# Kernel tuning notes

Hardware: AMD Instinct MI355X
Metric: run time of the kernel (lower is better)

The kernel has to match this reference:

```python
import jax, jax.numpy as jnp
import numpy as np

GRID = 0.5
NG = 48
NC = 16  # output channels
CHUNK = 256  # atoms per scan step (bounds peak memory)
E2 = float(np.exp(2.0))
# order matches pro_keys ['O','C','N','S'] with vdw_dic
VDW = jnp.array([1.52, 1.7, 1.55, 1.8], dtype=jnp.float32)


def setup_inputs() -> dict:
    key = jax.random.key(0)
    k1, k2, k3 = jax.random.split(key, 3)
    N = 2048
    coords = jax.random.uniform(k1, (N, 3), dtype=jnp.float32) * (NG * GRID)  # [0, 24)
    ch_idx = jax.random.randint(k2, (N,), 0, 4, dtype=jnp.int32)
    fg = jax.random.randint(k3, (N,), 0, 16, dtype=jnp.int32)
    return {"coords": coords, "ch_idx": ch_idx, "fg": fg}


def _channel_weights(ch_idx, fg):
    # base element channel 0..3
    w = jax.nn.one_hot(ch_idx, NC, dtype=jnp.float32)
    # fg routing: 14 -> +ch4 +ch5; 15 -> +ch6 +ch9; 12/13 -> nothing; else -> +ch(fg+4)
    c1 = jnp.where(fg == 14, 4, jnp.where(fg == 15, 6, fg + 4))
    c1 = jnp.where((fg == 12) | (fg == 13), -1, c1)  # one_hot(-1) == zeros
    c2 = jnp.where(fg == 14, 5, jnp.where(fg == 15, 9, -1))
    return w + jax.nn.one_hot(c1, NC, dtype=jnp.float32) + jax.nn.one_hot(c2, NC, dtype=jnp.float32)


def _grid_forward(coords, r, w):
    # coords [N,3], r [N] vdw radii, w [N,16] channel weights -> [16,48,48,48]
    gx = GRID * jnp.arange(NG, dtype=jnp.float32)  # grid point coordinates
    nchunk = coords.shape[0] // CHUNK
    coords_c = coords.reshape(nchunk, CHUNK, 3)
    r_c = r.reshape(nchunk, CHUNK)
    w_c = w.reshape(nchunk, CHUNK, NC)

    def body(acc, args):
        c, rr, ww = args  # [CHUNK,3], [CHUNK], [CHUNK,16]
        dx2 = (c[:, 0, None] - gx) ** 2  # [CHUNK,48]
        dy2 = (c[:, 1, None] - gx) ** 2
        dz2 = (c[:, 2, None] - gx) ** 2
        d2 = dx2[:, :, None, None] + dy2[:, None, :, None] + dz2[:, None, None, :]  # [CHUNK,48,48,48]
        d = jnp.sqrt(d2)
        r_ = rr[:, None, None, None]
        r2 = r_ * r_
        f1 = jnp.exp(-2.0 * d2 / r2)
        f2 = 4.0 * d2 / (E2 * r2) - 12.0 * d / (E2 * r_) + 9.0 / E2
        val = jnp.where(d < r_, f1, jnp.where(d < 1.5 * r_, f2, 0.0))
        acc = acc + jnp.einsum('nc,nxyz->cxyz', ww, val)
        return acc, None

    out, _ = jax.lax.scan(body, jnp.zeros((NC, NG, NG, NG), jnp.float32), (coords_c, r_c, w_c))
    return out


def reference(coords, ch_idx, fg):
    r = VDW[ch_idx]
    w = _channel_weights(ch_idx, fg)
    return _grid_forward(coords, r, w)
```

## Files before the change

### kernel.cpp

```cpp
#include <hip/hip_runtime.h>

#define NG 48
#define NC 16
#define NPTS (NG * NG * NG)
#define E2F 7.3890561f
#define NINE_OVER_E2 1.2180175f

#define BR 4
#define SEGCAP 48

__device__ __constant__ float c_vdw[4] = {1.52f, 1.7f, 1.55f, 1.8f};

__global__ void prep_kernel(const float* __restrict__ coords,
                            const int* __restrict__ ch_idx,
                            const int* __restrict__ fg,
                            float4* __restrict__ atomA,
                            float4* __restrict__ atomB, int natoms)
{
    const int i = blockIdx.x * blockDim.x + threadIdx.x;
    if (i >= natoms) return;
    const float x = coords[3 * i + 0];
    const float y = coords[3 * i + 1];
    const float z = coords[3 * i + 2];
    const int ci = ch_idx[i];
    const int f  = fg[i];
    const float r  = c_vdw[ci];
    const float r2 = r * r;
    int c1 = (f == 14) ? 4 : ((f == 15) ? 6 : f + 4);
    if (f == 12 || f == 13) c1 = -1;
    const int c2 = (f == 14) ? 5 : ((f == 15) ? 9 : -1);
    int mask = 1 << ci;
    if (c1 >= 0) mask |= 1 << c1;
    if (c2 >= 0) mask |= 1 << c2;
    atomA[i] = make_float4(x, y, z, 1.5f * r);
    atomB[i] = make_float4(-2.0f / r2, 4.0f / (E2F * r2),
                           12.0f / (E2F * r), __int_as_float(mask));
}

__global__ __launch_bounds__(256)
void density_kernel(const float4* __restrict__ atomA,
                    const float4* __restrict__ atomB,
                    float* __restrict__ out, int natoms)
{
    __shared__ float4 sA[4 * SEGCAP];
    __shared__ float4 sB[4 * SEGCAP];
    __shared__ int sCnt[4];
    __shared__ float sRed[4][NC][64];

    const int t = threadIdx.x;
    const int w = t >> 6;
    const int l = t & 63;
    const int bz = blockIdx.x, by = blockIdx.y, bx = blockIdx.z;

    const int tz = l & 3, ty = (l >> 2) & 3, tx = l >> 4;
    const int gx = bx * BR + tx, gy = by * BR + ty, gz = bz * BR + tz;
    const float px = gx * 0.5f, py = gy * 0.5f, pz = gz * 0.5f;

    const float blox = bx * 2.0f, bhix = blox + 1.5f;
    const float bloy = by * 2.0f, bhiy = bloy + 1.5f;
    const float bloz = bz * 2.0f, bhiz = bloz + 1.5f;

    const int quarter = (natoms + 3) >> 2;
    const int a0 = w * quarter;
    const int a1 = min(a0 + quarter, natoms);
    int myCnt = 0;
    for (int base = a0; base < a1; base += 64) {
        const int a = base + l;
        float4 pA;
        bool pred = false;
        if (a < a1) {
            pA = atomA[a];
            const float cut = pA.w;
            const float ddx = fmaxf(fmaxf(blox - pA.x, pA.x - bhix), 0.0f);
            const float ddy = fmaxf(fmaxf(bloy - pA.y, pA.y - bhiy), 0.0f);
            const float ddz = fmaxf(fmaxf(bloz - pA.z, pA.z - bhiz), 0.0f);
            pred = fmaf(ddx, ddx, fmaf(ddy, ddy, ddz * ddz)) < cut * cut;
        }
        const unsigned long long m = __ballot(pred);
        if (pred) {
            const int o = myCnt + __popcll(m & ((1ull << l) - 1ull));
            if (o < SEGCAP) {
                sA[w * SEGCAP + o] = pA;
                sB[w * SEGCAP + o] = atomB[a];
            }
        }
        myCnt += __popcll(m);
    }
    if (l == 0) sCnt[w] = (myCnt > SEGCAP) ? SEGCAP : myCnt;
    __syncthreads();

    const int c0 = sCnt[0], c1 = sCnt[1], c2 = sCnt[2], c3 = sCnt[3];

    float acc[NC];
    #pragma unroll
    for (int c = 0; c < NC; ++c) acc[c] = 0.0f;

    #pragma unroll 1
    for (int s = 0; s < 4; ++s) {
        const int cs = (s == 0) ? c0 : (s == 1) ? c1 : (s == 2) ? c2 : c3;
        const int segbase = s * SEGCAP;
        #pragma unroll 2
        for (int i = w; i < cs; i += 4) {
            const float4 A = sA[segbase + i];
            const float4 B = sB[segbase + i];
            const float dx = px - A.x;
            const float dy = py - A.y;
            const float dz = pz - A.z;
            const float d2 = fmaf(dx, dx, fmaf(dy, dy, dz * dz));
            const float cut2 = A.w * A.w;
            if (d2 < cut2) {
                const float r2 = cut2 * (4.0f / 9.0f);
                const float d  = sqrtf(d2);
                const float f1 = __expf(B.x * d2);
                const float f2 = fmaf(B.y, d2, fmaf(-B.z, d, NINE_OVER_E2));
                const float val = (d2 < r2) ? f1 : f2;
                const int chan = __builtin_amdgcn_readfirstlane(__float_as_int(B.w));
                #pragma unroll
                for (int c = 0; c < NC; ++c)
                    if (chan & (1 << c)) acc[c] += val;
            }
        }
    }

    #pragma unroll
    for (int c = 0; c < NC; ++c) sRed[w][c][l] = acc[c];
    __syncthreads();

    const int pbase = (gx * NG + gy) * NG + gz;
    #pragma unroll
    for (int k = 0; k < 4; ++k) {
        const int c = w * 4 + k;
        const float s = sRed[0][c][l] + sRed[1][c][l] +
                        sRed[2][c][l] + sRed[3][c][l];
        out[c * NPTS + pbase] = s;
    }
}

extern "C" void kernel_launch(void* const* d_in, const int* in_sizes, int n_in,
                              void* d_out, int out_size, void* d_ws, size_t ws_size,
                              hipStream_t stream) {
    (void)n_in; (void)ws_size; (void)out_size;
    const float* coords = (const float*)d_in[0];
    const int* ch = (const int*)d_in[1];
    const int* fgp = (const int*)d_in[2];
    float* out = (float*)d_out;
    const int natoms = in_sizes[0] / 3;

    float4* atomA = (float4*)d_ws;
    float4* atomB = atomA + natoms;

    prep_kernel<<<(natoms + 255) / 256, 256, 0, stream>>>(coords, ch, fgp, atomA, atomB, natoms);
    dim3 grid(NG / BR, NG / BR, NG / BR);
    density_kernel<<<grid, 256, 0, stream>>>(atomA, atomB, out, natoms);
}
```

Measured before the change: 23.50 us.

## Retile density kernel to 2x2x16 blocks with 8 waves and LDS atomic accumulation

Each block now covers a 2x2x16 grid-point tile, and 512 threads (8 waves) split the atom culling and the accumulation. Per-channel register accumulators are replaced by LDS atomicAdds into per-wave channel slots, applied only to the set bits of the channel mask. The per-atom distance branch becomes a select, and exp2 uses a constant prescaled by log2(e). The goal is cheaper accumulation and better occupancy. The cost is LDS atomic traffic, wasted math for atoms outside the cutoff, and a tighter SEGCAP that could truncate candidate lists for elongated tiles.

```diff
diff --git a/kernel.cpp b/kernel.cpp
--- a/kernel.cpp
+++ b/kernel.cpp
@@ -5,9 +5,10 @@
 #define NPTS (NG * NG * NG)
 #define E2F 7.3890561f
 #define NINE_OVER_E2 1.2180175f
+#define LOG2E 1.44269504f
 
-#define BR 4
-#define SEGCAP 48
+#define W 8
+#define SEGCAP 28
 
 __device__ __constant__ float c_vdw[4] = {1.52f, 1.7f, 1.55f, 1.8f};
 
@@ -33,74 +34,78 @@
     if (c1 >= 0) mask |= 1 << c1;
     if (c2 >= 0) mask |= 1 << c2;
     atomA[i] = make_float4(x, y, z, 1.5f * r);
-    atomB[i] = make_float4(-2.0f / r2, 4.0f / (E2F * r2),
-                           12.0f / (E2F * r), __int_as_float(mask));
+    atomB[i] = make_float4(-2.0f * LOG2E / r2,
+                           4.0f / (E2F * r2),
+                           12.0f / (E2F * r),
+                           __int_as_float(mask));
 }
 
-__global__ __launch_bounds__(256)
+__global__ __launch_bounds__(512, 8)
 void density_kernel(const float4* __restrict__ atomA,
                     const float4* __restrict__ atomB,
                     float* __restrict__ out, int natoms)
 {
-    __shared__ float4 sA[4 * SEGCAP];
-    __shared__ float4 sB[4 * SEGCAP];
-    __shared__ int sCnt[4];
-    __shared__ float sRed[4][NC][64];
+    __shared__ float4 sA[W * SEGCAP];
+    __shared__ float4 sB[W * SEGCAP];
+    __shared__ float sAcc[W][NC][64];
+    __shared__ int sCnt[W];
 
     const int t = threadIdx.x;
     const int w = t >> 6;
     const int l = t & 63;
     const int bz = blockIdx.x, by = blockIdx.y, bx = blockIdx.z;
 
-    const int tz = l & 3, ty = (l >> 2) & 3, tx = l >> 4;
-    const int gx = bx * BR + tx, gy = by * BR + ty, gz = bz * BR + tz;
-    const float px = gx * 0.5f, py = gy * 0.5f, pz = gz * 0.5f;
+    {
+        float4* p = (float4*)sAcc;
+        p[t]        = make_float4(0.f, 0.f, 0.f, 0.f);
+        p[t + 512]  = make_float4(0.f, 0.f, 0.f, 0.f);
+        p[t + 1024] = make_float4(0.f, 0.f, 0.f, 0.f);
+        p[t + 1536] = make_float4(0.f, 0.f, 0.f, 0.f);
+    }
 
-    const float blox = bx * 2.0f, bhix = blox + 1.5f;
-    const float bloy = by * 2.0f, bhiy = bloy + 1.5f;
-    const float bloz = bz * 2.0f, bhiz = bloz + 1.5f;
+    const float blox = bx * 1.0f, bhix = blox + 0.5f;
+    const float bloy = by * 1.0f, bhiy = bloy + 0.5f;
+    const float bloz = bz * 8.0f, bhiz = bloz + 7.5f;
 
-    const int quarter = (natoms + 3) >> 2;
-    const int a0 = w * quarter;
-    const int a1 = min(a0 + quarter, natoms);
-    int myCnt = 0;
+    const int chunk = (natoms + W - 1) / W;
+    const int a0 = w * chunk;
+    const int a1 = min(a0 + chunk, natoms);
+    int cnt = 0;
+    #pragma unroll 2
     for (int base = a0; base < a1; base += 64) {
         const int a = base + l;
         float4 pA;
         bool pred = false;
         if (a < a1) {
             pA = atomA[a];
-            const float cut = pA.w;
             const float ddx = fmaxf(fmaxf(blox - pA.x, pA.x - bhix), 0.0f);
             const float ddy = fmaxf(fmaxf(bloy - pA.y, pA.y - bhiy), 0.0f);
             const float ddz = fmaxf(fmaxf(bloz - pA.z, pA.z - bhiz), 0.0f);
-            pred = fmaf(ddx, ddx, fmaf(ddy, ddy, ddz * ddz)) < cut * cut;
+            pred = fmaf(ddx, ddx, fmaf(ddy, ddy, ddz * ddz)) < pA.w * pA.w;
         }
         const unsigned long long m = __ballot(pred);
         if (pred) {
-            const int o = myCnt + __popcll(m & ((1ull << l) - 1ull));
+            const int o = cnt + __popcll(m & ((1ull << l) - 1ull));
             if (o < SEGCAP) {
                 sA[w * SEGCAP + o] = pA;
                 sB[w * SEGCAP + o] = atomB[a];
             }
         }
-        myCnt += __popcll(m);
+        cnt += __popcll(m);
     }
-    if (l == 0) sCnt[w] = (myCnt > SEGCAP) ? SEGCAP : myCnt;
+    if (l == 0) sCnt[w] = (cnt > SEGCAP) ? SEGCAP : cnt;
     __syncthreads();
 
-    const int c0 = sCnt[0], c1 = sCnt[1], c2 = sCnt[2], c3 = sCnt[3];
+    const int tz = l & 15, ty = (l >> 4) & 1, tx = l >> 5;
+    const float px = (bx * 2 + tx) * 0.5f;
+    const float py = (by * 2 + ty) * 0.5f;
+    const float pz = (bz * 16 + tz) * 0.5f;
 
-    float acc[NC];
-    #pragma unroll
-    for (int c = 0; c < NC; ++c) acc[c] = 0.0f;
-
-    #pragma unroll 1
-    for (int s = 0; s < 4; ++s) {
-        const int cs = (s == 0) ? c0 : (s == 1) ? c1 : (s == 2) ? c2 : c3;
+    float* const accw = &sAcc[w][0][l];
+    for (int s = 0; s < W; ++s) {
+        const int cs = sCnt[s];
         const int segbase = s * SEGCAP;
-        #pragma unroll 2
-        for (int i = w; i < cs; i += 4) {
+        for (int i = (w + s) & 7; i < cs; i += W) {
             const float4 A = sA[segbase + i];
             const float4 B = sB[segbase + i];
             const float dx = px - A.x;
@@ -108,31 +113,41 @@
             const float dz = pz - A.z;
             const float d2 = fmaf(dx, dx, fmaf(dy, dy, dz * dz));
             const float cut2 = A.w * A.w;
-            if (d2 < cut2) {
-                const float r2 = cut2 * (4.0f / 9.0f);
-                const float d  = sqrtf(d2);
-                const float f1 = __expf(B.x * d2);
-                const float f2 = fmaf(B.y, d2, fmaf(-B.z, d, NINE_OVER_E2));
-                const float val = (d2 < r2) ? f1 : f2;
-                const int chan = __builtin_amdgcn_readfirstlane(__float_as_int(B.w));
-                #pragma unroll
-                for (int c = 0; c < NC; ++c)
-                    if (chan & (1 << c)) acc[c] += val;
+            const float r2 = cut2 * (4.0f / 9.0f);
+            const float d  = sqrtf(d2);
+            const float f1 = exp2f(B.x * d2);
+            const float f2 = fmaf(B.y, d2, fmaf(-B.z, d, NINE_OVER_E2));
+            float val = (d2 < r2) ? f1 : f2;
+            val = (d2 < cut2) ? val : 0.0f;
+            int chan = __builtin_amdgcn_readfirstlane(__float_as_int(B.w));
+            int c0 = __builtin_ctz(chan);
+            atomicAdd(accw + c0 * 64, val);
+            chan &= chan - 1;
+            if (chan) {
+                const int c1 = __builtin_ctz(chan);
+                atomicAdd(accw + c1 * 64, val);
+                chan &= chan - 1;
+                if (chan) {
+                    const int c2 = __builtin_ctz(chan);
+                    atomicAdd(accw + c2 * 64, val);
+                }
             }
         }
     }
+    __syncthreads();
 
     #pragma unroll
-    for (int c = 0; c < NC; ++c) sRed[w][c][l] = acc[c];
-    __syncthreads();
-
-    const int pbase = (gx * NG + gy) * NG + gz;
-    #pragma unroll
-    for (int k = 0; k < 4; ++k) {
-        const int c = w * 4 + k;
-        const float s = sRed[0][c][l] + sRed[1][c][l] +
-                        sRed[2][c][l] + sRed[3][c][l];
-        out[c * NPTS + pbase] = s;
+    for (int j = 0; j < 2; ++j) {
+        const int idx = t + j * 512;
+        const int c  = idx >> 6;
+        const int ll = idx & 63;
+        float sum = 0.0f;
+        #pragma unroll
+        for (int s = 0; s < W; ++s) sum += sAcc[s][c][ll];
+        const int gz = bz * 16 + (ll & 15);
+        const int gy = by * 2 + ((ll >> 4) & 1);
+        const int gx = bx * 2 + (ll >> 5);
+        out[c * NPTS + (gx * NG + gy) * NG + gz] = sum;
     }
 }
 
@@ -150,6 +165,6 @@
     float4* atomB = atomA + natoms;
 
     prep_kernel<<<(natoms + 255) / 256, 256, 0, stream>>>(coords, ch, fgp, atomA, atomB, natoms);
-    dim3 grid(NG / BR, NG / BR, NG / BR);
-    density_kernel<<<grid, 256, 0, stream>>>(atomA, atomB, out, natoms);
+    dim3 grid(NG / 16, NG / 2, NG / 2);
+    density_kernel<<<grid, 512, 0, stream>>>(atomA, atomB, out, natoms);
 }
```

Result: slower. 61.96 us (+163.7%).

## Bin atoms into 27 super-block lists so density blocks scan few candidates

Applied to the files above, without the earlier changes.

Adds a build kernel that computes atom parameters and bins atoms into 27 spatial super-blocks (8 Å cubes, with cutoff overlap), each capped at 512 entries. Density blocks then scan only their super-block's list instead of all 2048 atoms, which cuts global loads and the cull work per block. It also folds log2(e) into the exponent coefficient so exp2f can be used, and reuses the staging shared memory as the reduction buffer. Risks are silent truncation if a super-block holds more than 512 atoms, and a build kernel of only 27 blocks that re-reads all atoms in each block.

```diff
diff --git a/kernel.cpp b/kernel.cpp
--- a/kernel.cpp
+++ b/kernel.cpp
@@ -5,91 +5,150 @@
 #define NPTS (NG * NG * NG)
 #define E2F 7.3890561f
 #define NINE_OVER_E2 1.2180175f
+#define LOG2E 1.44269504f
 
 #define BR 4
 #define SEGCAP 48
+#define SBCAP 512
+#define MAXATOMS 2048
 
 __device__ __constant__ float c_vdw[4] = {1.52f, 1.7f, 1.55f, 1.8f};
 
-__global__ void prep_kernel(const float* __restrict__ coords,
-                            const int* __restrict__ ch_idx,
-                            const int* __restrict__ fg,
-                            float4* __restrict__ atomA,
-                            float4* __restrict__ atomB, int natoms)
-{
-    const int i = blockIdx.x * blockDim.x + threadIdx.x;
-    if (i >= natoms) return;
-    const float x = coords[3 * i + 0];
-    const float y = coords[3 * i + 1];
-    const float z = coords[3 * i + 2];
-    const int ci = ch_idx[i];
-    const int f  = fg[i];
-    const float r  = c_vdw[ci];
+__device__ __forceinline__ void atom_params(int ci, int f, float r,
+                                            float& b0, float& b1, float& b2, int& mask) {
     const float r2 = r * r;
     int c1 = (f == 14) ? 4 : ((f == 15) ? 6 : f + 4);
     if (f == 12 || f == 13) c1 = -1;
     const int c2 = (f == 14) ? 5 : ((f == 15) ? 9 : -1);
-    int mask = 1 << ci;
+    mask = 1 << ci;
     if (c1 >= 0) mask |= 1 << c1;
     if (c2 >= 0) mask |= 1 << c2;
-    atomA[i] = make_float4(x, y, z, 1.5f * r);
-    atomB[i] = make_float4(-2.0f / r2, 4.0f / (E2F * r2),
-                           12.0f / (E2F * r), __int_as_float(mask));
+    b0 = -2.0f * LOG2E / r2;
+    b1 = 4.0f / (E2F * r2);
+    b2 = 12.0f / (E2F * r);
+}
+
+__global__ __launch_bounds__(1024)
+void build_kernel(const float* __restrict__ coords,
+                  const int* __restrict__ ch_idx,
+                  const int* __restrict__ fg,
+                  float4* __restrict__ segA, float4* __restrict__ segB,
+                  int* __restrict__ counts, int natoms)
+{
+    __shared__ float sx[MAXATOMS], sy[MAXATOMS], sz[MAXATOMS], scut[MAXATOMS];
+    __shared__ float sb0[MAXATOMS], sb1[MAXATOMS], sb2[MAXATOMS], sb3[MAXATOMS];
+    __shared__ int sCnt[16];
+
+    const int t = threadIdx.x, w = t >> 6, l = t & 63;
+    const int n = min(natoms, MAXATOMS);
+
+    for (int i = t; i < n; i += 1024) {
+        const float x = coords[3 * i], y = coords[3 * i + 1], z = coords[3 * i + 2];
+        const int ci = ch_idx[i], f = fg[i];
+        const float r = c_vdw[ci];
+        float b0, b1, b2; int mask;
+        atom_params(ci, f, r, b0, b1, b2, mask);
+        sx[i] = x; sy[i] = y; sz[i] = z; scut[i] = 1.5f * r;
+        sb0[i] = b0; sb1[i] = b1; sb2[i] = b2; sb3[i] = __int_as_float(mask);
+    }
+    __syncthreads();
+
+    const int sb = blockIdx.x;
+    const int sbx = sb / 9, sby = (sb / 3) % 3, sbz = sb % 3;
+    const float lox = sbx * 8.0f, hix = lox + 7.5f;
+    const float loy = sby * 8.0f, hiy = loy + 7.5f;
+    const float loz = sbz * 8.0f, hiz = loz + 7.5f;
+
+    int runTot = 0;
+    for (int base = 0; base < n; base += 1024) {
+        const int a = base + t;
+        bool pred = false;
+        float ax = 0.f, ay = 0.f, az = 0.f, cut = 0.f;
+        if (a < n) {
+            ax = sx[a]; ay = sy[a]; az = sz[a]; cut = scut[a];
+            const float ddx = fmaxf(fmaxf(lox - ax, ax - hix), 0.f);
+            const float ddy = fmaxf(fmaxf(loy - ay, ay - hiy), 0.f);
+            const float ddz = fmaxf(fmaxf(loz - az, az - hiz), 0.f);
+            pred = fmaf(ddx, ddx, fmaf(ddy, ddy, ddz * ddz)) < cut * cut;
+        }
+        const unsigned long long m = __ballot(pred);
+        if (l == 0) sCnt[w] = __popcll(m);
+        __syncthreads();
+        int ofs = runTot, tot = 0;
+        #pragma unroll
+        for (int w2 = 0; w2 < 16; ++w2) {
+            const int c = sCnt[w2];
+            if (w2 < w) ofs += c;
+            tot += c;
+        }
+        if (pred) {
+            const int o = ofs + __popcll(m & ((1ull << l) - 1ull));
+            if (o < SBCAP) {
+                segA[sb * SBCAP + o] = make_float4(ax, ay, az, cut);
+                segB[sb * SBCAP + o] = make_float4(sb0[a], sb1[a], sb2[a], sb3[a]);
+            }
+        }
+        runTot += tot;
+        __syncthreads();
+    }
+    if (t == 0) counts[sb] = min(runTot, SBCAP);
 }
 
 __global__ __launch_bounds__(256)
-void density_kernel(const float4* __restrict__ atomA,
-                    const float4* __restrict__ atomB,
-                    float* __restrict__ out, int natoms)
+void density_kernel(const float4* __restrict__ segA,
+                    const float4* __restrict__ segB,
+                    const int* __restrict__ counts,
+                    float* __restrict__ out)
 {
-    __shared__ float4 sA[4 * SEGCAP];
-    __shared__ float4 sB[4 * SEGCAP];
+    __shared__ __align__(16) unsigned char smem[16384];
     __shared__ int sCnt[4];
-    __shared__ float sRed[4][NC][64];
-
-    const int t = threadIdx.x;
-    const int w = t >> 6;
-    const int l = t & 63;
+    float4* const sA = (float4*)smem;
+    float4* const sB = sA + 4 * SEGCAP;
+    float (*const sRed)[64] = (float (*)[64])smem;
+
+    const int t = threadIdx.x, w = t >> 6, l = t & 63;
     const int bz = blockIdx.x, by = blockIdx.y, bx = blockIdx.z;
-
-    const int tz = l & 3, ty = (l >> 2) & 3, tx = l >> 4;
-    const int gx = bx * BR + tx, gy = by * BR + ty, gz = bz * BR + tz;
-    const float px = gx * 0.5f, py = gy * 0.5f, pz = gz * 0.5f;
 
     const float blox = bx * 2.0f, bhix = blox + 1.5f;
     const float bloy = by * 2.0f, bhiy = bloy + 1.5f;
     const float bloz = bz * 2.0f, bhiz = bloz + 1.5f;
 
-    const int quarter = (natoms + 3) >> 2;
-    const int a0 = w * quarter;
-    const int a1 = min(a0 + quarter, natoms);
+    const int sb = ((bx >> 2) * 3 + (by >> 2)) * 3 + (bz >> 2);
+    const int cnt_sb = counts[sb];
+    const float4* const srcA = segA + sb * SBCAP;
+    const float4* const srcB = segB + sb * SBCAP;
+
+    const int q = (cnt_sb + 3) >> 2;
+    const int i0 = w * q, i1 = min(i0 + q, cnt_sb);
     int myCnt = 0;
-    for (int base = a0; base < a1; base += 64) {
-        const int a = base + l;
-        float4 pA;
+    for (int base = i0; base < i1; base += 64) {
+        const int idx = base + l;
         bool pred = false;
-        if (a < a1) {
-            pA = atomA[a];
-            const float cut = pA.w;
-            const float ddx = fmaxf(fmaxf(blox - pA.x, pA.x - bhix), 0.0f);
-            const float ddy = fmaxf(fmaxf(bloy - pA.y, pA.y - bhiy), 0.0f);
-            const float ddz = fmaxf(fmaxf(bloz - pA.z, pA.z - bhiz), 0.0f);
-            pred = fmaf(ddx, ddx, fmaf(ddy, ddy, ddz * ddz)) < cut * cut;
+        float4 pA, pB;
+        if (idx < i1) {
+            pA = srcA[idx];
+            pB = srcB[idx];
+            const float ddx = fmaxf(fmaxf(blox - pA.x, pA.x - bhix), 0.f);
+            const float ddy = fmaxf(fmaxf(bloy - pA.y, pA.y - bhiy), 0.f);
+            const float ddz = fmaxf(fmaxf(bloz - pA.z, pA.z - bhiz), 0.f);
+            pred = fmaf(ddx, ddx, fmaf(ddy, ddy, ddz * ddz)) < pA.w * pA.w;
         }
         const unsigned long long m = __ballot(pred);
         if (pred) {
             const int o = myCnt + __popcll(m & ((1ull << l) - 1ull));
-            if (o < SEGCAP) {
-                sA[w * SEGCAP + o] = pA;
-                sB[w * SEGCAP + o] = atomB[a];
-            }
+            if (o < SEGCAP) { sA[w * SEGCAP + o] = pA; sB[w * SEGCAP + o] = pB; }
         }
         myCnt += __popcll(m);
     }
-    if (l == 0) sCnt[w] = (myCnt > SEGCAP) ? SEGCAP : myCnt;
+    if (l == 0) sCnt[w] = min(myCnt, SEGCAP);
     __syncthreads();
 
     const int c0 = sCnt[0], c1 = sCnt[1], c2 = sCnt[2], c3 = sCnt[3];
+
+    const int tz = l & 3, ty = (l >> 2) & 3, tx = l >> 4;
+    const float px = (bx * BR + tx) * 0.5f;
+    const float py = (by * BR + ty) * 0.5f;
+    const float pz = (bz * BR + tz) * 0.5f;
 
     float acc[NC];
     #pragma unroll
@@ -111,7 +170,7 @@
             if (d2 < cut2) {
                 const float r2 = cut2 * (4.0f / 9.0f);
                 const float d  = sqrtf(d2);
-                const float f1 = __expf(B.x * d2);
+                const float f1 = exp2f(B.x * d2);
                 const float f2 = fmaf(B.y, d2, fmaf(-B.z, d, NINE_OVER_E2));
                 const float val = (d2 < r2) ? f1 : f2;
                 const int chan = __builtin_amdgcn_readfirstlane(__float_as_int(B.w));
@@ -121,35 +180,152 @@
             }
         }
     }
-
-    #pragma unroll
-    for (int c = 0; c < NC; ++c) sRed[w][c][l] = acc[c];
-    __syncthreads();
-
+    __syncthreads();
+
+    #pragma unroll
+    for (int c = 0; c < NC; ++c) sRed[w * NC + c][l] = acc[c];
+    __syncthreads();
+
+    const int gx = bx * BR + tx, gy = by * BR + ty, gz = bz * BR + tz;
     const int pbase = (gx * NG + gy) * NG + gz;
     #pragma unroll
     for (int k = 0; k < 4; ++k) {
         const int c = w * 4 + k;
-        const float s = sRed[0][c][l] + sRed[1][c][l] +
-                        sRed[2][c][l] + sRed[3][c][l];
+        const float s = sRed[0 * NC + c][l] + sRed[1 * NC + c][l] +
+                        sRed[2 * NC + c][l] + sRed[3 * NC + c][l];
         out[c * NPTS + pbase] = s;
+    }
+}
+
+__global__ void prep_kernel(const float* __restrict__ coords,
+                            const int* __restrict__ ch_idx,
+                            const int* __restrict__ fg,
+                            float4* __restrict__ atomA,
+                            float4* __restrict__ atomB, int natoms)
+{
+    const int i = blockIdx.x * blockDim.x + threadIdx.x;
+    if (i >= natoms) return;
+    const int ci = ch_idx[i], f = fg[i];
+    const float r = c_vdw[ci];
+    float b0, b1, b2; int mask;
+    atom_params(ci, f, r, b0, b1, b2, mask);
+    atomA[i] = make_float4(coords[3 * i], coords[3 * i + 1], coords[3 * i + 2], 1.5f * r);
+    atomB[i] = make_float4(b0, b1, b2, __int_as_float(mask));
+}
+
+__global__ __launch_bounds__(256)
+void density_scan_kernel(const float4* __restrict__ atomA,
+                         const float4* __restrict__ atomB,
+                         float* __restrict__ out, int natoms)
+{
+    __shared__ __align__(16) unsigned char smem[16384];
+    __shared__ int sCnt[4];
+    float4* const sA = (float4*)smem;
+    float4* const sB = sA + 4 * SEGCAP;
+    float (*const sRed)[64] = (float (*)[64])smem;
+
+    const int t = threadIdx.x, w = t >> 6, l = t & 63;
+    const int bz = blockIdx.x, by = blockIdx.y, bx = blockIdx.z;
+
+    const float blox = bx * 2.0f, bhix = blox + 1.5f;
+    const float bloy = by * 2.0f, bhiy = bloy + 1.5f;
+    const float bloz = bz * 2.0f, bhiz = bloz + 1.5f;
+
+    const int quarter = (natoms + 3) >> 2;
+    const int a0 = w * quarter, a1 = min(a0 + quarter, natoms);
+    int myCnt = 0;
+    for (int base = a0; base < a1; base += 64) {
+        const int a = base + l;
+        bool pred = false; float4 pA;
+        if (a < a1) {
+            pA = atomA[a];
+            const float ddx = fmaxf(fmaxf(blox - pA.x, pA.x - bhix), 0.f);
+            const float ddy = fmaxf(fmaxf(bloy - pA.y, pA.y - bhiy), 0.f);
+            const float ddz = fmaxf(fmaxf(bloz - pA.z, pA.z - bhiz), 0.f);
+            pred = fmaf(ddx, ddx, fmaf(ddy, ddy, ddz * ddz)) < pA.w * pA.w;
+        }
+        const unsigned long long m = __ballot(pred);
+        if (pred) {
+            const int o = myCnt + __popcll(m & ((1ull << l) - 1ull));
+            if (o < SEGCAP) { sA[w * SEGCAP + o] = pA; sB[w * SEGCAP + o] = atomB[a]; }
+        }
+        myCnt += __popcll(m);
+    }
+    if (l == 0) sCnt[w] = min(myCnt, SEGCAP);
+    __syncthreads();
+
+    const int c0 = sCnt[0], c1 = sCnt[1], c2 = sCnt[2], c3 = sCnt[3];
+    const int tz = l & 3, ty = (l >> 2) & 3, tx = l >> 4;
+    const float px = (bx * BR + tx) * 0.5f;
+    const float py = (by * BR + ty) * 0.5f;
+    const float pz = (bz * BR + tz) * 0.5f;
+
+    float acc[NC];
+    #pragma unroll
+    for (int c = 0; c < NC; ++c) acc[c] = 0.0f;
+
+    #pragma unroll 1
+    for (int s = 0; s < 4; ++s) {
+        const int cs = (s == 0) ? c0 : (s == 1) ? c1 : (s == 2) ? c2 : c3;
+        const int segbase = s * SEGCAP;
+        #pragma unroll 2
+        for (int i = w; i < cs; i += 4) {
+            const float4 A = sA[segbase + i];
+            const float4 B = sB[segbase + i];
+            const float dx = px - A.x, dy = py - A.y, dz = pz - A.z;
+            const float d2 = fmaf(dx, dx, fmaf(dy, dy, dz * dz));
+            const float cut2 = A.w * A.w;
+            if (d2 < cut2) {
+                const float r2 = cut2 * (4.0f / 9.0f);
+                const float d  = sqrtf(d2);
+                const float f1 = exp2f(B.x * d2);
+                const float f2 = fmaf(B.y, d2, fmaf(-B.z, d, NINE_OVER_E2));
+                const float val = (d2 < r2) ? f1 : f2;
+                const int chan = __builtin_amdgcn_readfirstlane(__float_as_int(B.w));
+                #pragma unroll
+                for (int c = 0; c < NC; ++c)
+                    if (chan & (1 << c)) acc[c] += val;
+            }
+        }
+    }
+    __syncthreads();
+    #pragma unroll
+    for (int c = 0; c < NC; ++c) sRed[w * NC + c][l] = acc[c];
+    __syncthreads();
+
+    const int gx = bx * BR + tx, gy = by * BR + ty, gz = bz * BR + tz;
+    const int pbase = (gx * NG + gy) * NG + gz;
+    #pragma unroll
+    for (int k = 0; k < 4; ++k) {
+        const int c = w * 4 + k;
+        out[c * NPTS + pbase] = sRed[0 * NC + c][l] + sRed[1 * NC + c][l] +
+                                sRed[2 * NC + c][l] + sRed[3 * NC + c][l];
     }
 }
 
 extern "C" void kernel_launch(void* const* d_in, const int* in_sizes, int n_in,
                               void* d_out, int out_size, void* d_ws, size_t ws_size,
                               hipStream_t stream) {
-    (void)n_in; (void)ws_size; (void)out_size;
+    (void)n_in; (void)out_size;
     const float* coords = (const float*)d_in[0];
     const int* ch = (const int*)d_in[1];
     const int* fgp = (const int*)d_in[2];
     float* out = (float*)d_out;
     const int natoms = in_sizes[0] / 3;
 
-    float4* atomA = (float4*)d_ws;
-    float4* atomB = atomA + natoms;
-
-    prep_kernel<<<(natoms + 255) / 256, 256, 0, stream>>>(coords, ch, fgp, atomA, atomB, natoms);
+    const size_t need = 256 + 2ull * 27 * SBCAP * sizeof(float4);
     dim3 grid(NG / BR, NG / BR, NG / BR);
-    density_kernel<<<grid, 256, 0, stream>>>(atomA, atomB, out, natoms);
-}
+
+    if (natoms <= MAXATOMS && ws_size >= need) {
+        int* counts = (int*)d_ws;
+        float4* segA = (float4*)((char*)d_ws + 256);
+        float4* segB = segA + 27 * SBCAP;
+        build_kernel<<<27, 1024, 0, stream>>>(coords, ch, fgp, segA, segB, counts, natoms);
+        density_kernel<<<grid, 256, 0, stream>>>(segA, segB, counts, out);
+    } else {
+        float4* atomA = (float4*)d_ws;
+        float4* atomB = atomA + natoms;
+        prep_kernel<<<(natoms + 255) / 256, 256, 0, stream>>>(coords, ch, fgp, atomA, atomB, natoms);
+        density_scan_kernel<<<grid, 256, 0, stream>>>(atomA, atomB, out, natoms);
+    }
+}
```

After: 21.39 us (median of 2 runs). -9.0%, faster.

## Fuse atom prep into density kernel with larger per-block tiles

Applied to the files above, without the earlier changes.

Removes the separate prep kernel and derives atom parameters inside the density kernel's culling pass, so one launch does the work and the workspace round trip is gone. Each block now covers a 4x4x16 voxel tile with one voxel per thread, and every thread loops over all culled atoms, which drops the cross-wave shared-memory reduction. The distance branch becomes branchless masked FMAs and exp is computed via exp2. The trade-off is that every block rescans all atoms for fewer, larger blocks, each thread evaluates every candidate atom, and the per-wave segment cap grows to 64, which could drop atoms if a larger tile sees more.

```diff
diff --git a/kernel.cpp b/kernel.cpp
--- a/kernel.cpp
+++ b/kernel.cpp
@@ -4,92 +4,85 @@
 #define NC 16
 #define NPTS (NG * NG * NG)
 #define E2F 7.3890561f
-#define NINE_OVER_E2 1.2180175f
+#define NINE_OVER_E2 1.2180176f
+#define LOG2E 1.44269504f
 
-#define BR 4
-#define SEGCAP 48
+#define SEGCAP 64
 
-__device__ __constant__ float c_vdw[4] = {1.52f, 1.7f, 1.55f, 1.8f};
-
-__global__ void prep_kernel(const float* __restrict__ coords,
-                            const int* __restrict__ ch_idx,
-                            const int* __restrict__ fg,
-                            float4* __restrict__ atomA,
-                            float4* __restrict__ atomB, int natoms)
-{
-    const int i = blockIdx.x * blockDim.x + threadIdx.x;
-    if (i >= natoms) return;
-    const float x = coords[3 * i + 0];
-    const float y = coords[3 * i + 1];
-    const float z = coords[3 * i + 2];
-    const int ci = ch_idx[i];
-    const int f  = fg[i];
-    const float r  = c_vdw[ci];
-    const float r2 = r * r;
+__device__ __forceinline__ float sel_r(int ci) {
+    return ci == 0 ? 1.52f : ci == 1 ? 1.7f : ci == 2 ? 1.55f : 1.8f;
+}
+__device__ __forceinline__ int chan_mask(int ci, int f) {
     int c1 = (f == 14) ? 4 : ((f == 15) ? 6 : f + 4);
     if (f == 12 || f == 13) c1 = -1;
     const int c2 = (f == 14) ? 5 : ((f == 15) ? 9 : -1);
     int mask = 1 << ci;
     if (c1 >= 0) mask |= 1 << c1;
     if (c2 >= 0) mask |= 1 << c2;
-    atomA[i] = make_float4(x, y, z, 1.5f * r);
-    atomB[i] = make_float4(-2.0f / r2, 4.0f / (E2F * r2),
-                           12.0f / (E2F * r), __int_as_float(mask));
+    return mask;
 }
 
 __global__ __launch_bounds__(256)
-void density_kernel(const float4* __restrict__ atomA,
-                    const float4* __restrict__ atomB,
-                    float* __restrict__ out, int natoms)
+void density_fused_kernel(const float* __restrict__ coords,
+                          const int* __restrict__ ch_idx,
+                          const int* __restrict__ fg,
+                          float* __restrict__ out, int natoms)
 {
     __shared__ float4 sA[4 * SEGCAP];
     __shared__ float4 sB[4 * SEGCAP];
     __shared__ int sCnt[4];
-    __shared__ float sRed[4][NC][64];
 
-    const int t = threadIdx.x;
-    const int w = t >> 6;
-    const int l = t & 63;
+    const int t = threadIdx.x, w = t >> 6, l = t & 63;
     const int bz = blockIdx.x, by = blockIdx.y, bx = blockIdx.z;
 
-    const int tz = l & 3, ty = (l >> 2) & 3, tx = l >> 4;
-    const int gx = bx * BR + tx, gy = by * BR + ty, gz = bz * BR + tz;
-    const float px = gx * 0.5f, py = gy * 0.5f, pz = gz * 0.5f;
-
-    const float blox = bx * 2.0f, bhix = blox + 1.5f;
-    const float bloy = by * 2.0f, bhiy = bloy + 1.5f;
-    const float bloz = bz * 2.0f, bhiz = bloz + 1.5f;
+    const float lox = bx * 2.0f, hix = lox + 1.5f;
+    const float loy = by * 2.0f, hiy = loy + 1.5f;
+    const float loz = bz * 8.0f, hiz = loz + 7.5f;
 
     const int quarter = (natoms + 3) >> 2;
     const int a0 = w * quarter;
     const int a1 = min(a0 + quarter, natoms);
-    int myCnt = 0;
+    int cnt = 0;
+    #pragma unroll 2
     for (int base = a0; base < a1; base += 64) {
         const int a = base + l;
-        float4 pA;
         bool pred = false;
+        float ax = 0.f, ay = 0.f, az = 0.f, r = 1.f, cut = 0.f;
+        int ci = 0;
         if (a < a1) {
-            pA = atomA[a];
-            const float cut = pA.w;
-            const float ddx = fmaxf(fmaxf(blox - pA.x, pA.x - bhix), 0.0f);
-            const float ddy = fmaxf(fmaxf(bloy - pA.y, pA.y - bhiy), 0.0f);
-            const float ddz = fmaxf(fmaxf(bloz - pA.z, pA.z - bhiz), 0.0f);
+            ax = coords[3 * a]; ay = coords[3 * a + 1]; az = coords[3 * a + 2];
+            ci = ch_idx[a];
+            r = sel_r(ci);
+            cut = 1.5f * r;
+            const float ddx = fmaxf(fmaxf(lox - ax, ax - hix), 0.f);
+            const float ddy = fmaxf(fmaxf(loy - ay, ay - hiy), 0.f);
+            const float ddz = fmaxf(fmaxf(loz - az, az - hiz), 0.f);
             pred = fmaf(ddx, ddx, fmaf(ddy, ddy, ddz * ddz)) < cut * cut;
         }
         const unsigned long long m = __ballot(pred);
         if (pred) {
-            const int o = myCnt + __popcll(m & ((1ull << l) - 1ull));
+            const int o = cnt + __popcll(m & ((1ull << l) - 1ull));
             if (o < SEGCAP) {
-                sA[w * SEGCAP + o] = pA;
-                sB[w * SEGCAP + o] = atomB[a];
+                const float r2 = r * r;
+                const int f = fg[a];
+                sA[w * SEGCAP + o] = make_float4(ax, ay, az, cut);
+                sB[w * SEGCAP + o] = make_float4(-2.0f * LOG2E / r2,
+                                                 4.0f / (E2F * r2),
+                                                 12.0f / (E2F * r),
+                                                 __int_as_float(chan_mask(ci, f)));
             }
         }
-        myCnt += __popcll(m);
+        cnt += __popcll(m);
     }
-    if (l == 0) sCnt[w] = (myCnt > SEGCAP) ? SEGCAP : myCnt;
+    if (l == 0) sCnt[w] = min(cnt, SEGCAP);
     __syncthreads();
 
     const int c0 = sCnt[0], c1 = sCnt[1], c2 = sCnt[2], c3 = sCnt[3];
+
+    const int tz = t & 15, ty = (t >> 4) & 3, tx = t >> 6;
+    const float px = (bx * 4 + tx) * 0.5f;
+    const float py = (by * 4 + ty) * 0.5f;
+    const float pz = (bz * 16 + tz) * 0.5f;
 
     float acc[NC];
     #pragma unroll
@@ -100,7 +93,7 @@
         const int cs = (s == 0) ? c0 : (s == 1) ? c1 : (s == 2) ? c2 : c3;
         const int segbase = s * SEGCAP;
         #pragma unroll 2
-        for (int i = w; i < cs; i += 4) {
+        for (int i = 0; i < cs; ++i) {
             const float4 A = sA[segbase + i];
             const float4 B = sB[segbase + i];
             const float dx = px - A.x;
@@ -108,48 +101,38 @@
             const float dz = pz - A.z;
             const float d2 = fmaf(dx, dx, fmaf(dy, dy, dz * dz));
             const float cut2 = A.w * A.w;
-            if (d2 < cut2) {
-                const float r2 = cut2 * (4.0f / 9.0f);
-                const float d  = sqrtf(d2);
-                const float f1 = __expf(B.x * d2);
-                const float f2 = fmaf(B.y, d2, fmaf(-B.z, d, NINE_OVER_E2));
-                const float val = (d2 < r2) ? f1 : f2;
-                const int chan = __builtin_amdgcn_readfirstlane(__float_as_int(B.w));
-                #pragma unroll
-                for (int c = 0; c < NC; ++c)
-                    if (chan & (1 << c)) acc[c] += val;
+            const float r2 = cut2 * (4.0f / 9.0f);
+            const float d  = sqrtf(d2);
+            const float f1 = exp2f(B.x * d2);
+            const float f2 = fmaf(B.y, d2, fmaf(-B.z, d, NINE_OVER_E2));
+            float val = (d2 < r2) ? f1 : f2;
+            val = (d2 < cut2) ? val : 0.0f;
+            const int chan = __builtin_amdgcn_readfirstlane(__float_as_int(B.w));
+            #pragma unroll
+            for (int c = 0; c < NC; ++c) {
+                const float msk = __int_as_float(((chan >> c) & 1) * 0x3f800000);
+                acc[c] = fmaf(msk, val, acc[c]);
             }
         }
     }
 
-    #pragma unroll
-    for (int c = 0; c < NC; ++c) sRed[w][c][l] = acc[c];
-    __syncthreads();
-
+    const int gx = bx * 4 + tx, gy = by * 4 + ty, gz = bz * 16 + tz;
     const int pbase = (gx * NG + gy) * NG + gz;
     #pragma unroll
-    for (int k = 0; k < 4; ++k) {
-        const int c = w * 4 + k;
-        const float s = sRed[0][c][l] + sRed[1][c][l] +
-                        sRed[2][c][l] + sRed[3][c][l];
-        out[c * NPTS + pbase] = s;
-    }
+    for (int c = 0; c < NC; ++c)
+        out[c * NPTS + pbase] = acc[c];
 }
 
 extern "C" void kernel_launch(void* const* d_in, const int* in_sizes, int n_in,
                               void* d_out, int out_size, void* d_ws, size_t ws_size,
                               hipStream_t stream) {
-    (void)n_in; (void)ws_size; (void)out_size;
+    (void)n_in; (void)out_size; (void)d_ws; (void)ws_size;
     const float* coords = (const float*)d_in[0];
     const int* ch = (const int*)d_in[1];
     const int* fgp = (const int*)d_in[2];
     float* out = (float*)d_out;
     const int natoms = in_sizes[0] / 3;
 
-    float4* atomA = (float4*)d_ws;
-    float4* atomB = atomA + natoms;
-
-    prep_kernel<<<(natoms + 255) / 256, 256, 0, stream>>>(coords, ch, fgp, atomA, atomB, natoms);
-    dim3 grid(NG / BR, NG / BR, NG / BR);
-    density_kernel<<<grid, 256, 0, stream>>>(atomA, atomB, out, natoms);
+    dim3 grid(NG / 16, NG / 4, NG / 4);
+    density_fused_kernel<<<grid, 256, 0, stream>>>(coords, ch, fgp, out, natoms);
 }
```

Result: slower. 32.60 us (+38.7%).
